# Optimization experiments

Hardware: AMD Instinct MI355X
Metric: run time of the kernel (lower is better)

## Reference

```python
import jax, jax.numpy as jnp
import numpy as np

N, C, T, V = 8, 256, 256, 25
NH = 8
DK = 256           # dk_factor(1.0) * out_channels
DV = 256           # only_temporal_attention -> dv = out_channels
DKH = DK // NH     # 32
DVH = DV // NH     # 32
BN_EPS = 1e-5


def setup_inputs() -> dict:
    key = jax.random.key(0)
    ks = jax.random.split(key, 10)
    return {
        "x": jax.random.normal(ks[0], (N, C, T, V), jnp.float32),
        # pointwise (1,1) qkv conv: weight (2*dk+dv, C), torch conv_init scale
        "qkv_w": jax.random.normal(ks[1], (2 * DK + DV, C), jnp.float32) * (2.0 / (2 * DK + DV)) ** 0.5,
        "qkv_b": jax.random.normal(ks[2], (2 * DK + DV,), jnp.float32) * 0.02,
        # relative key embeddings: (2*frames-1, dk // Nh)
        "key_rel": jax.random.normal(ks[3], (2 * T - 1, DKH), jnp.float32),
        # attn_out pointwise conv: (dv, dv)
        "attn_w": jax.random.normal(ks[4], (DV, DV), jnp.float32) * (1.0 / DV) ** 0.5,
        "attn_b": jax.random.normal(ks[5], (DV,), jnp.float32) * 0.02,
        # BatchNorm2d (eval mode) params / running stats
        "bn_gamma": 1.0 + 0.1 * jax.random.normal(ks[6], (DV,), jnp.float32),
        "bn_beta": 0.1 * jax.random.normal(ks[7], (DV,), jnp.float32),
        "bn_mean": 0.1 * jax.random.normal(ks[8], (DV,), jnp.float32),
        "bn_var": jax.random.uniform(ks[9], (DV,), jnp.float32, minval=0.5, maxval=1.5),
    }


def rel_to_abs(x):
    # x: (B, Nh, L, 2L-1) -> (B, Nh, L, L) via standard pad/reshape/slice trick
    B, Nh, L, _ = x.shape
    x = jnp.pad(x, ((0, 0), (0, 0), (0, 0), (0, 1)))          # (B,Nh,L,2L)
    flat = x.reshape(B, Nh, L * 2 * L)
    flat = jnp.pad(flat, ((0, 0), (0, 0), (0, L - 1)))
    final = flat.reshape(B, Nh, L + 1, 2 * L - 1)
    return final[:, :, :L, L - 1:]


def reference(x, qkv_w, qkv_b, key_rel, attn_w, attn_b, bn_gamma, bn_beta, bn_mean, bn_var):
    n, c, t, v = x.shape
    x_sum = x
    B = n * v
    # (N,C,T,V) -> (N*V, C, T): each joint is an independent temporal sequence
    xr = jnp.transpose(x, (0, 3, 1, 2)).reshape(B, c, t)
    # pointwise qkv conv (kernel (1,1), stride 1)
    qkv = jnp.einsum('bct,oc->bot', xr, qkv_w) + qkv_b[None, :, None]
    q, k, vv = qkv[:, :DK], qkv[:, DK:2 * DK], qkv[:, 2 * DK:]
    q = q.reshape(B, NH, DKH, t) * (DKH ** -0.5)   # scaling applied before rel logits too
    k = k.reshape(B, NH, DKH, t)
    vv = vv.reshape(B, NH, DVH, t)
    # content logits: (B,NH,t,t)
    logits = jnp.einsum('bhdt,bhds->bhts', q, k)
    # relative logits: (B,NH,t,2t-1) -> abs (B,NH,t,t)
    rel = jnp.einsum('bhdt,md->bhtm', q, key_rel)
    logits = logits + rel_to_abs(rel)
    weights = jax.nn.softmax(logits, axis=-1)
    attn = jnp.einsum('bhts,bhds->bhtd', weights, vv)          # (B,NH,t,DVH)
    # combine heads (head-major channel order) -> (B, DV, t)
    attn = jnp.transpose(attn, (0, 1, 3, 2)).reshape(B, DV, t)
    # attn_out pointwise conv
    attn = jnp.einsum('bct,oc->bot', attn, attn_w) + attn_b[None, :, None]
    # (N*V, DV, T) -> (N, DV, T, V)
    attn = attn.reshape(n, v, DV, t).transpose(0, 2, 3, 1)
    # skip connection (in==out, stride==1 -> identity down path)
    result = attn + x_sum
    # BatchNorm2d in eval mode
    inv = bn_gamma / jnp.sqrt(bn_var + BN_EPS)
    result = result * inv[None, :, None, None] + (bn_beta - bn_mean * inv)[None, :, None, None]
    return jax.nn.relu(result)
```

## Files before the change

### kernel.cpp

```cpp
#include <hip/hip_runtime.h>

#define NB 8
#define CC 256
#define TT 256
#define VV 25

typedef unsigned int u32;
typedef unsigned short u16;
typedef __attribute__((ext_vector_type(8))) short s16x8;
typedef __attribute__((ext_vector_type(4))) float f32x4;

__device__ __forceinline__ float bf2f(u16 u) { return __uint_as_float((u32)u << 16); }
__device__ __forceinline__ u16 f2bf(float f) {
    u32 u = __float_as_uint(f);
    u += 0x7fffu + ((u >> 16) & 1u);
    return (u16)(u >> 16);
}

__device__ __forceinline__ void gload_lds16(const void* g, void* l) {
    __builtin_amdgcn_global_load_lds(
        (const __attribute__((address_space(1))) u32*)g,
        (__attribute__((address_space(3))) u32*)l, 16, 0, 0);
}

__global__ __launch_bounds__(256) void k_transpose_x(const float* __restrict__ x,
                                                     u16* __restrict__ xT) {
    __shared__ u16 L[25 * 32 * 34];
    const int tid = threadIdx.x;
    const int c0 = blockIdx.x * 32;
    const int t0 = blockIdx.y * 32;
    const int n  = blockIdx.z;
    for (int i = tid; i < 25600; i += 256) {
        int ci = i / 800;
        int rem = i - ci * 800;
        int t = rem / 25;
        int v = rem - t * 25;
        float f = x[(((size_t)(n * CC + c0 + ci)) * TT + t0) * VV + rem];
        L[(v * 32 + t) * 34 + ci] = f2bf(f);
    }
    __syncthreads();
    for (int i = tid; i < 12800; i += 256) {
        int row = i >> 4, cp = i & 15;
        int v = row >> 5, t = row & 31;
        u32 val = *(const u32*)&L[row * 34 + cp * 2];
        *(u32*)&xT[(((size_t)(n * VV + v)) * TT + t0 + t) * CC + c0 + cp * 2] = val;
    }
}

__global__ __launch_bounds__(256) void k_pack_krel(const float* __restrict__ kr,
                                                   u16* __restrict__ krb) {
    int g = blockIdx.x * 256 + threadIdx.x;
    if (g >= 16384) return;
    krb[g] = (g < 511 * 32) ? f2bf(kr[g]) : (u16)0;
}

__global__ __launch_bounds__(256) void k_pack_w(const float* __restrict__ qkv_w,
                                                const float* __restrict__ attn_w,
                                                const float* __restrict__ qkv_b,
                                                u16* __restrict__ Wqk,
                                                u16* __restrict__ Wv,
                                                u16* __restrict__ Wo,
                                                float* __restrict__ bqk) {
    const float s = 0.17677669529663687f;
    int g = blockIdx.x * 256 + threadIdx.x;
    if (g < 131072) {
        Wqk[g] = f2bf(qkv_w[g] * (g < 65536 ? s : 1.f));
    } else if (g < 196608) {
        Wv[g - 131072] = f2bf(qkv_w[g]);
    } else if (g < 262144) {
        Wo[g - 196608] = f2bf(attn_w[g - 196608]);
    } else if (g < 262656) {
        int i = g - 262144;
        bqk[i] = qkv_b[i] * (i < 256 ? s : 1.f);
    }
}

__device__ __forceinline__ void gemm_mainloop(const u16* __restrict__ Arow,
                                              const u16* __restrict__ Brow,
                                              u16* At, u16* Bt,
                                              int wave, int lane, f32x4 acc[4][4]) {
    const int srow = lane >> 2, scol = (lane & 3) * 8;
    const int quad = lane >> 4, l15 = lane & 15;
    for (int k0 = 0; k0 < 256; k0 += 32) {
#pragma unroll
        for (int it = 0; it < 2; ++it) {
            int ch = it * 4 + wave;
            gload_lds16(Arow + (size_t)(ch * 16 + srow) * 256 + k0 + scol, At + ch * 512 + lane * 8);
            gload_lds16(Brow + (size_t)(ch * 16 + srow) * 256 + k0 + scol, Bt + ch * 512 + lane * 8);
        }
        __syncthreads();
        s16x8 af[4], bfr[4];
#pragma unroll
        for (int i = 0; i < 4; ++i)
            af[i] = *(const s16x8*)&At[((wave & 1) * 64 + i * 16 + l15) * 32 + quad * 8];
#pragma unroll
        for (int j = 0; j < 4; ++j)
            bfr[j] = *(const s16x8*)&Bt[((wave >> 1) * 64 + j * 16 + l15) * 32 + quad * 8];
#pragma unroll
        for (int i = 0; i < 4; ++i)
#pragma unroll
            for (int j = 0; j < 4; ++j)
                acc[i][j] = __builtin_amdgcn_mfma_f32_16x16x32_bf16(af[i], bfr[j], acc[i][j], 0, 0, 0);
        __syncthreads();
    }
}

__global__ __launch_bounds__(256) void k_gemm_qk(const u16* __restrict__ xT,
                                                 const u16* __restrict__ Wqk,
                                                 const float* __restrict__ bqk,
                                                 u16* __restrict__ qT,
                                                 u16* __restrict__ kT) {
    __shared__ __align__(16) u16 At[128 * 32];
    __shared__ __align__(16) u16 Bt[128 * 32];
    const int tid = threadIdx.x, wave = tid >> 6, lane = tid & 63;
    const int quad = lane >> 4, l15 = lane & 15;
    const int n0 = blockIdx.x * 128;
    const int m0 = blockIdx.y * 128;
    const int b  = blockIdx.z;
    const u16* Arow = xT + (size_t)b * 65536 + (size_t)m0 * 256;
    const u16* Brow = Wqk + (size_t)n0 * 256;
    f32x4 acc[4][4];
#pragma unroll
    for (int i = 0; i < 4; ++i)
#pragma unroll
        for (int j = 0; j < 4; ++j) acc[i][j] = (f32x4){0.f, 0.f, 0.f, 0.f};
    gemm_mainloop(Arow, Brow, At, Bt, wave, lane, acc);

    const bool isq = (n0 < 256);
    u16* base = isq ? qT : kT;
    const int on0 = (isq ? n0 : n0 - 256) + (wave >> 1) * 64;
#pragma unroll
    for (int j = 0; j < 4; ++j) {
        int o = on0 + j * 16 + l15;
        float bias = bqk[(isq ? 0 : 256) + o];
        u16* dcol = base + (size_t)(b * 8 + (o >> 5)) * 8192 + (o & 31);
#pragma unroll
        for (int i = 0; i < 4; ++i) {
            int tbase = m0 + (wave & 1) * 64 + i * 16 + quad * 4;
#pragma unroll
            for (int r = 0; r < 4; ++r)
                dcol[(size_t)(tbase + r) * 32] = f2bf(acc[i][j][r] + bias);
        }
    }
}

__global__ __launch_bounds__(256) void k_gemm_av(const u16* __restrict__ Wb,
                                                 const float* __restrict__ bias,
                                                 const u16* __restrict__ Bsrc,
                                                 u16* __restrict__ Out) {
    __shared__ __align__(16) u16 At[128 * 32];
    __shared__ __align__(16) u16 Bt[128 * 32];
    const int tid = threadIdx.x, wave = tid >> 6, lane = tid & 63;
    const int quad = lane >> 4, l15 = lane & 15;
    const int n0 = blockIdx.x * 128;
    const int m0 = blockIdx.y * 128;
    const int b  = blockIdx.z;
    const u16* Arow = Wb + (size_t)m0 * 256;
    const u16* Brow = Bsrc + (size_t)b * 65536 + (size_t)n0 * 256;
    f32x4 acc[4][4];
#pragma unroll
    for (int i = 0; i < 4; ++i)
#pragma unroll
        for (int j = 0; j < 4; ++j) acc[i][j] = (f32x4){0.f, 0.f, 0.f, 0.f};
    gemm_mainloop(Arow, Brow, At, Bt, wave, lane, acc);

    u16* ob = Out + (size_t)b * 65536;
    const int nb = n0 + (wave >> 1) * 64 + l15;
#pragma unroll
    for (int i = 0; i < 4; ++i) {
        int o_i = m0 + (wave & 1) * 64 + i * 16 + quad * 4;
#pragma unroll
        for (int r = 0; r < 4; ++r) {
            float bv = bias[o_i + r];
            u16* orow = ob + (size_t)(o_i + r) * 256 + nb;
#pragma unroll
            for (int j = 0; j < 4; ++j)
                orow[j * 16] = f2bf(acc[i][j][r] + bv);
        }
    }
}

__global__ __launch_bounds__(256) void k_attention_mfma(const u16* __restrict__ qT,
                                                        const u16* __restrict__ kT,
                                                        const u16* __restrict__ vb,
                                                        const u16* __restrict__ krb,
                                                        u16* __restrict__ attn) {
    __shared__ __align__(16) u16 RP[4][16 * 280];

    const int tid = threadIdx.x;
    const int bh = blockIdx.x;
    const int b = bh >> 3, h = bh & 7;
    const int wave = tid >> 6, lane = tid & 63;
    const int quad = lane >> 4, l15 = lane & 15;
    const int t0w = blockIdx.y * 64 + wave * 16;
    const int tl = quad * 4;

    u16* rp = &RP[wave][0];
    const u16* qg  = qT  + (size_t)bh * 8192;
    const u16* kg  = kT  + (size_t)bh * 8192;
    const u16* vg  = vb  + (size_t)bh * 8192;
    const u16* krg = krb + (size_t)(240 - t0w) * 32;

    s16x8 afrag = *(const s16x8*)(qg + (size_t)(t0w + l15) * 32 + quad * 8);

#pragma unroll
    for (int j = 0; j < 17; ++j) {
        s16x8 bfrag = *(const s16x8*)(krg + (size_t)(j * 16 + l15) * 32 + quad * 8);
        f32x4 c = {0.f, 0.f, 0.f, 0.f};
        c = __builtin_amdgcn_mfma_f32_16x16x32_bf16(afrag, bfrag, c, 0, 0, 0);
        int col = j * 16 + l15;
        rp[(tl + 0) * 280 + col] = f2bf(c[0]);
        rp[(tl + 1) * 280 + col] = f2bf(c[1]);
        rp[(tl + 2) * 280 + col] = f2bf(c[2]);
        rp[(tl + 3) * 280 + col] = f2bf(c[3]);
    }

    f32x4 acc[16];
#pragma unroll
    for (int n = 0; n < 16; ++n) {
        s16x8 kf = *(const s16x8*)(kg + (size_t)(n * 16 + l15) * 32 + quad * 8);
        f32x4 z = {0.f, 0.f, 0.f, 0.f};
        acc[n] = __builtin_amdgcn_mfma_f32_16x16x32_bf16(afrag, kf, z, 0, 0, 0);
    }
#pragma unroll
    for (int n = 0; n < 16; ++n) {
#pragma unroll
        for (int r = 0; r < 4; ++r) {
            int tlr = tl + r;
            acc[n][r] += bf2f(rp[tlr * 280 + (n * 16 + l15 - tlr + 15)]);
        }
    }
    float invr[4];
#pragma unroll
    for (int r = 0; r < 4; ++r) {
        float m = acc[0][r];
#pragma unroll
        for (int n = 1; n < 16; ++n) m = fmaxf(m, acc[n][r]);
#pragma unroll
        for (int off = 1; off < 16; off <<= 1) m = fmaxf(m, __shfl_xor(m, off, 64));
        float s = 0.f;
#pragma unroll
        for (int n = 0; n < 16; ++n) {
            float e = __expf(acc[n][r] - m);
            acc[n][r] = e;
            s += e;
        }
#pragma unroll
        for (int off = 1; off < 16; off <<= 1) s += __shfl_xor(s, off, 64);
        invr[r] = 1.f / s;
    }
#pragma unroll
    for (int n = 0; n < 16; ++n) {
#pragma unroll
        for (int r = 0; r < 4; ++r)
            rp[(tl + r) * 280 + n * 16 + l15] = f2bf(acc[n][r] * invr[r]);
    }

#pragma unroll
    for (int j = 0; j < 2; ++j) {
        f32x4 o = {0.f, 0.f, 0.f, 0.f};
#pragma unroll
        for (int ks = 0; ks < 8; ++ks) {
            s16x8 a  = *(const s16x8*)&rp[l15 * 280 + ks * 32 + quad * 8];
            s16x8 bv = *(const s16x8*)(vg + (size_t)(j * 16 + l15) * 256 + ks * 32 + quad * 8);
            o = __builtin_amdgcn_mfma_f32_16x16x32_bf16(a, bv, o, 0, 0, 0);
        }
        u16* ob = attn + ((size_t)b * 256 + t0w + tl) * 256 + h * 32 + j * 16 + l15;
        ob[0]   = f2bf(o[0]);
        ob[256] = f2bf(o[1]);
        ob[512] = f2bf(o[2]);
        ob[768] = f2bf(o[3]);
    }
}

__global__ __launch_bounds__(256) void k_final(const u16* __restrict__ y,
                                               const float* __restrict__ x,
                                               const float* __restrict__ gamma,
                                               const float* __restrict__ beta,
                                               const float* __restrict__ mean,
                                               const float* __restrict__ var,
                                               float* __restrict__ out) {
    __shared__ float tile[1600];
    const int tid = threadIdx.x;
    const int t0 = blockIdx.x * 64;
    const int o  = blockIdx.y;
    const int n  = blockIdx.z;
    float inv = gamma[o] * rsqrtf(var[o] + 1e-5f);
    float sh  = beta[o] - mean[o] * inv;
    for (int p = tid; p < 1600; p += 256) {
        int v = p >> 6, j = p & 63;
        tile[j * VV + v] = bf2f(y[(((size_t)(n * VV + v)) * CC + o) * TT + t0 + j]);
    }
    __syncthreads();
    size_t gbase = (((size_t)(n * CC + o)) * TT + t0) * VV;
    for (int i = tid; i < 1600; i += 256) {
        float val = tile[i] + x[gbase + i];
        val = val * inv + sh;
        out[gbase + i] = fmaxf(val, 0.f);
    }
}

extern "C" void kernel_launch(void* const* d_in, const int* in_sizes, int n_in,
                              void* d_out, int out_size, void* d_ws, size_t ws_size,
                              hipStream_t stream) {
    const float* x        = (const float*)d_in[0];
    const float* qkv_w    = (const float*)d_in[1];
    const float* qkv_b    = (const float*)d_in[2];
    const float* key_rel  = (const float*)d_in[3];
    const float* attn_w   = (const float*)d_in[4];
    const float* attn_b   = (const float*)d_in[5];
    const float* bn_gamma = (const float*)d_in[6];
    const float* bn_beta  = (const float*)d_in[7];
    const float* bn_mean  = (const float*)d_in[8];
    const float* bn_var   = (const float*)d_in[9];
    float* out = (float*)d_out;

    char* ws = (char*)d_ws;
    u16* xT    = (u16*)ws;
    u16* qT    = (u16*)(ws + 26214400);
    u16* kT    = (u16*)(ws + 52428800);
    u16* vb    = (u16*)(ws + 78643200);
    u16* attnT = (u16*)(ws + 104857600);
    u16* y     = qT;

    char* outc = (char*)d_out;
    u16* Wqk   = (u16*)outc;
    u16* Wv    = (u16*)(outc + 262144);
    u16* Wo    = (u16*)(outc + 393216);
    float* bqk = (float*)(outc + 524288);
    u16* krb   = (u16*)(outc + 526336);

    k_pack_w<<<1026, 256, 0, stream>>>(qkv_w, attn_w, qkv_b, Wqk, Wv, Wo, bqk);
    k_pack_krel<<<64, 256, 0, stream>>>(key_rel, krb);
    k_transpose_x<<<dim3(8, 8, 8), 256, 0, stream>>>(x, xT);
    k_gemm_qk<<<dim3(4, 2, 200), 256, 0, stream>>>(xT, Wqk, bqk, qT, kT);
    k_gemm_av<<<dim3(2, 2, 200), 256, 0, stream>>>(Wv, qkv_b + 512, xT, vb);
    k_attention_mfma<<<dim3(1600, 4), 256, 0, stream>>>(qT, kT, vb, krb, attnT);
    k_gemm_av<<<dim3(2, 2, 200), 256, 0, stream>>>(Wo, attn_b, attnT, y);
    k_final<<<dim3(4, 256, 8), 256, 0, stream>>>(y, x, bn_gamma, bn_beta, bn_mean, bn_var, out);
}
```

Measured before the change: 346.7 us.

## Compute relative logits in registers via shuffles, use exp2 and XCD-aware block mapping

Replaces the LDS round-trip for relative-position logits with MFMA results shifted directly between lanes using __shfl. The bf16 rounding of the rel logits is also removed. Folds log2(e) into the q weight scale so the softmax can use exp2f. Normalization is deferred to the PV output. The grid is flattened and remapped so that blocks sharing a (b,h) land on the same XCD for L2 reuse, and s_setprio hints and a launch-bounds occupancy target are added. The aim is to cut LDS traffic, instruction count and cache misses in the attention kernel, at the cost of more shuffle instructions and a different rounding path.

New measurement: 347.1 us. About the same (+0.1%).

```diff
diff --git a/kernel.cpp b/kernel.cpp
--- a/kernel.cpp
+++ b/kernel.cpp
@@ -1,4 +1,5 @@
 #include <hip/hip_runtime.h>
+#include <stdint.h>
 
 #define NB 8
 #define CC 256
@@ -61,7 +62,7 @@
                                                 u16* __restrict__ Wv,
                                                 u16* __restrict__ Wo,
                                                 float* __restrict__ bqk) {
-    const float s = 0.17677669529663687f;
+    const float s = 0.17677669529663687f * 1.4426950408889634f;
     int g = blockIdx.x * 256 + threadIdx.x;
     if (g < 131072) {
         Wqk[g] = f2bf(qkv_w[g] * (g < 65536 ? s : 1.f));
@@ -180,19 +181,23 @@
     }
 }
 
-__global__ __launch_bounds__(256) void k_attention_mfma(const u16* __restrict__ qT,
-                                                        const u16* __restrict__ kT,
-                                                        const u16* __restrict__ vb,
-                                                        const u16* __restrict__ krb,
-                                                        u16* __restrict__ attn) {
+__global__ __launch_bounds__(256, 4) void k_attention_mfma(const u16* __restrict__ qT,
+                                                           const u16* __restrict__ kT,
+                                                           const u16* __restrict__ vb,
+                                                           const u16* __restrict__ krb,
+                                                           u16* __restrict__ attn) {
     __shared__ __align__(16) u16 RP[4][16 * 280];
 
     const int tid = threadIdx.x;
-    const int bh = blockIdx.x;
+    const int bx = blockIdx.x;
+    const int xcd = bx & 7;
+    const int ii  = bx >> 3;
+    const int bh  = xcd * 200 + (ii >> 2);
+    const int tt  = ii & 3;
     const int b = bh >> 3, h = bh & 7;
     const int wave = tid >> 6, lane = tid & 63;
     const int quad = lane >> 4, l15 = lane & 15;
-    const int t0w = blockIdx.y * 64 + wave * 16;
+    const int t0w = tt * 64 + wave * 16;
     const int tl = quad * 4;
 
     u16* rp = &RP[wave][0];
@@ -202,74 +207,87 @@
     const u16* krg = krb + (size_t)(240 - t0w) * 32;
 
     s16x8 afrag = *(const s16x8*)(qg + (size_t)(t0w + l15) * 32 + quad * 8);
-
-#pragma unroll
-    for (int j = 0; j < 17; ++j) {
-        s16x8 bfrag = *(const s16x8*)(krg + (size_t)(j * 16 + l15) * 32 + quad * 8);
-        f32x4 c = {0.f, 0.f, 0.f, 0.f};
-        c = __builtin_amdgcn_mfma_f32_16x16x32_bf16(afrag, bfrag, c, 0, 0, 0);
-        int col = j * 16 + l15;
-        rp[(tl + 0) * 280 + col] = f2bf(c[0]);
-        rp[(tl + 1) * 280 + col] = f2bf(c[1]);
-        rp[(tl + 2) * 280 + col] = f2bf(c[2]);
-        rp[(tl + 3) * 280 + col] = f2bf(c[3]);
-    }
+    const f32x4 z4 = {0.f, 0.f, 0.f, 0.f};
 
     f32x4 acc[16];
+    __builtin_amdgcn_s_setprio(1);
 #pragma unroll
     for (int n = 0; n < 16; ++n) {
         s16x8 kf = *(const s16x8*)(kg + (size_t)(n * 16 + l15) * 32 + quad * 8);
-        f32x4 z = {0.f, 0.f, 0.f, 0.f};
-        acc[n] = __builtin_amdgcn_mfma_f32_16x16x32_bf16(afrag, kf, z, 0, 0, 0);
-    }
+        acc[n] = __builtin_amdgcn_mfma_f32_16x16x32_bf16(afrag, kf, z4, 0, 0, 0);
+    }
+    __builtin_amdgcn_s_setprio(0);
+
+    int srcl[4];
+    bool msrc[4];
+#pragma unroll
+    for (int r = 0; r < 4; ++r) {
+        int K = 15 - tl - r;
+        srcl[r] = quad * 16 + ((l15 + K) & 15);
+        msrc[r] = l15 < K;
+    }
+    f32x4 rc = __builtin_amdgcn_mfma_f32_16x16x32_bf16(
+        afrag, *(const s16x8*)(krg + (size_t)l15 * 32 + quad * 8), z4, 0, 0, 0);
 #pragma unroll
     for (int n = 0; n < 16; ++n) {
+        f32x4 rn = __builtin_amdgcn_mfma_f32_16x16x32_bf16(
+            afrag, *(const s16x8*)(krg + (size_t)((n + 1) * 16 + l15) * 32 + quad * 8),
+            z4, 0, 0, 0);
 #pragma unroll
         for (int r = 0; r < 4; ++r) {
-            int tlr = tl + r;
-            acc[n][r] += bf2f(rp[tlr * 280 + (n * 16 + l15 - tlr + 15)]);
-        }
-    }
+            float vsel = msrc[r] ? rn[r] : rc[r];
+            acc[n][r] += __shfl(vsel, srcl[r], 64);
+        }
+        rc = rn;
+    }
+
     float invr[4];
 #pragma unroll
     for (int r = 0; r < 4; ++r) {
-        float m = acc[0][r];
-#pragma unroll
-        for (int n = 1; n < 16; ++n) m = fmaxf(m, acc[n][r]);
+        float mr[8];
+#pragma unroll
+        for (int n = 0; n < 8; ++n) mr[n] = fmaxf(acc[n][r], acc[n + 8][r]);
+#pragma unroll
+        for (int n = 0; n < 4; ++n) mr[n] = fmaxf(mr[n], mr[n + 4]);
+        float m = fmaxf(fmaxf(mr[0], mr[1]), fmaxf(mr[2], mr[3]));
 #pragma unroll
         for (int off = 1; off < 16; off <<= 1) m = fmaxf(m, __shfl_xor(m, off, 64));
-        float s = 0.f;
-#pragma unroll
-        for (int n = 0; n < 16; ++n) {
-            float e = __expf(acc[n][r] - m);
-            acc[n][r] = e;
-            s += e;
-        }
+#pragma unroll
+        for (int n = 0; n < 16; ++n) acc[n][r] = exp2f(acc[n][r] - m);
+        float sr[8];
+#pragma unroll
+        for (int n = 0; n < 8; ++n) sr[n] = acc[n][r] + acc[n + 8][r];
+#pragma unroll
+        for (int n = 0; n < 4; ++n) sr[n] = sr[n] + sr[n + 4];
+        float s = (sr[0] + sr[1]) + (sr[2] + sr[3]);
 #pragma unroll
         for (int off = 1; off < 16; off <<= 1) s += __shfl_xor(s, off, 64);
         invr[r] = 1.f / s;
     }
+
 #pragma unroll
     for (int n = 0; n < 16; ++n) {
 #pragma unroll
         for (int r = 0; r < 4; ++r)
-            rp[(tl + r) * 280 + n * 16 + l15] = f2bf(acc[n][r] * invr[r]);
+            rp[(tl + r) * 280 + n * 16 + l15] = f2bf(acc[n][r]);
     }
 
 #pragma unroll
     for (int j = 0; j < 2; ++j) {
         f32x4 o = {0.f, 0.f, 0.f, 0.f};
+        __builtin_amdgcn_s_setprio(1);
 #pragma unroll
         for (int ks = 0; ks < 8; ++ks) {
             s16x8 a  = *(const s16x8*)&rp[l15 * 280 + ks * 32 + quad * 8];
             s16x8 bv = *(const s16x8*)(vg + (size_t)(j * 16 + l15) * 256 + ks * 32 + quad * 8);
             o = __builtin_amdgcn_mfma_f32_16x16x32_bf16(a, bv, o, 0, 0, 0);
         }
+        __builtin_amdgcn_s_setprio(0);
         u16* ob = attn + ((size_t)b * 256 + t0w + tl) * 256 + h * 32 + j * 16 + l15;
-        ob[0]   = f2bf(o[0]);
-        ob[256] = f2bf(o[1]);
-        ob[512] = f2bf(o[2]);
-        ob[768] = f2bf(o[3]);
+        ob[0]   = f2bf(o[0] * invr[0]);
+        ob[256] = f2bf(o[1] * invr[1]);
+        ob[512] = f2bf(o[2] * invr[2]);
+        ob[768] = f2bf(o[3] * invr[3]);
     }
 }
 
@@ -335,7 +353,7 @@
     k_transpose_x<<<dim3(8, 8, 8), 256, 0, stream>>>(x, xT);
     k_gemm_qk<<<dim3(4, 2, 200), 256, 0, stream>>>(xT, Wqk, bqk, qT, kT);
     k_gemm_av<<<dim3(2, 2, 200), 256, 0, stream>>>(Wv, qkv_b + 512, xT, vb);
-    k_attention_mfma<<<dim3(1600, 4), 256, 0, stream>>>(qT, kT, vb, krb, attnT);
+    k_attention_mfma<<<dim3(6400), 256, 0, stream>>>(qT, kT, vb, krb, attnT);
     k_gemm_av<<<dim3(2, 2, 200), 256, 0, stream>>>(Wo, attn_b, attnT, y);
     k_final<<<dim3(4, 256, 8), 256, 0, stream>>>(y, x, bn_gamma, bn_beta, bn_mean, bn_var, out);
 }
```
